# Kernel tuning notes

Measured on AMD Instinct MI355X. Metric: run time of the kernel, lower is better.

Reference implementation:

```python
import jax, jax.numpy as jnp
import numpy as np

# ---- static config (matches init_kwargs) ----
D_MODEL = 2048
D_STATE = 64
D_CONV = 4
EXPAND = 2
HEADDIM = 64
NGROUPS = 1
CHUNK = 256
D_INNER = EXPAND * D_MODEL            # 4096
NHEADS = D_INNER // HEADDIM           # 64
CONV_DIM = D_INNER + 2 * NGROUPS * D_STATE   # 4224
D_IN_PROJ = 2 * D_INNER + 2 * NGROUPS * D_STATE + NHEADS  # 8384
EPS = 1e-5


def setup_inputs() -> dict:
    key = jax.random.key(0)
    ks = jax.random.split(key, 7)
    B, L = 2, 2048
    u = jax.random.normal(ks[0], (B, L, D_MODEL), jnp.float32)
    W_in = jax.random.normal(ks[1], (D_IN_PROJ, D_MODEL), jnp.float32) * (D_MODEL ** -0.5)
    conv_w = jax.random.normal(ks[2], (CONV_DIM, D_CONV), jnp.float32) * (D_CONV ** -0.5)
    conv_b = jnp.zeros((CONV_DIM,), jnp.float32)
    # dt_bias = softplus^{-1}(dt) with dt ~ LogUniform(1e-3, 1e-1), as in the torch init
    dt = jnp.exp(jax.random.uniform(ks[3], (NHEADS,), jnp.float32)
                 * (np.log(0.1) - np.log(0.001)) + np.log(0.001))
    dt_bias = dt + jnp.log(-jnp.expm1(-dt))
    A_log = jnp.log(jax.random.uniform(ks[4], (NHEADS,), jnp.float32, minval=1.0, maxval=16.0))
    D = jnp.ones((NHEADS,), jnp.float32)
    norm_w = jnp.ones((D_INNER,), jnp.float32)
    W_out = jax.random.normal(ks[5], (D_MODEL, D_INNER), jnp.float32) * (D_INNER ** -0.5)
    return dict(u=u, W_in=W_in, conv_w=conv_w, conv_b=conv_b, dt_bias=dt_bias,
                A_log=A_log, D=D, norm_w=norm_w, W_out=W_out)


def _chunked_ssd(x, dt, A, Bm, Cm):
    """Mamba2 chunked selective scan (ssd, discrete form).
    x:[b,l,h,p] dt:[b,l,h] A:[h] Bm,Cm:[b,l,n] (ngroups=1, broadcast over heads).
    Returns y:[b,l,h,p]."""
    b, l, h, p = x.shape
    c = l // CHUNK
    xc = x.reshape(b, c, CHUNK, h, p)
    dtc = dt.reshape(b, c, CHUNK, h)
    Bc = Bm.reshape(b, c, CHUNK, D_STATE)
    Cc = Cm.reshape(b, c, CHUNK, D_STATE)

    Abar = (dtc * A).transpose(0, 3, 1, 2)          # [b,h,c,s]
    Acum = jnp.cumsum(Abar, axis=-1)                # [b,h,c,s]

    # intra-chunk decay matrix L[i,j] = exp(sum_{k=j+1..i} Abar_k), lower-tri
    seg = Acum[..., :, None] - Acum[..., None, :]   # [b,h,c,s,s]
    tri = jnp.tril(jnp.ones((CHUNK, CHUNK), bool))
    Lmat = jnp.where(tri, jnp.exp(seg), 0.0)

    xdt = xc * dtc[..., None]                       # [b,c,s,h,p] (dt*B*x discretization)
    Y_diag = jnp.einsum('bcln,bcsn,bhcls,bcshp->bclhp', Cc, Bc, Lmat, xdt)

    # per-chunk final states
    decay_states = jnp.exp(Acum[..., -1:] - Acum)   # [b,h,c,s]
    states = jnp.einsum('bcsn,bhcs,bcshp->bchpn', Bc, decay_states, xdt)

    # inter-chunk recurrence (associative scan across chunk summaries)
    Achunk = Acum[..., -1]                          # [b,h,c]
    Acs = jnp.cumsum(jnp.pad(Achunk, ((0, 0), (0, 0), (1, 0))), axis=-1)  # [b,h,c+1]
    segc = Acs[..., :, None] - Acs[..., None, :]
    tric = jnp.tril(jnp.ones((c + 1, c + 1), bool))
    decay_chunk = jnp.where(tric, jnp.exp(segc), 0.0)          # [b,h,c+1,c+1]
    states0 = jnp.pad(states, ((0, 0), (1, 0), (0, 0), (0, 0), (0, 0)))  # zero init state
    new_states = jnp.einsum('bhzc,bchpn->bzhpn', decay_chunk, states0)
    prev_states = new_states[:, :-1]                # state entering each chunk [b,c,h,p,n]

    state_decay = jnp.exp(Acum)                     # [b,h,c,s]
    Y_off = jnp.einsum('bcln,bchpn,bhcl->bclhp', Cc, prev_states, state_decay)
    return (Y_diag + Y_off).reshape(b, l, h, p)


def reference(u, W_in, conv_w, conv_b, dt_bias, A_log, D, norm_w, W_out):
    b, l, _ = u.shape
    zxbcdt = u @ W_in.T                                        # [b,l,8384]
    z = zxbcdt[..., :D_INNER]
    xBC = zxbcdt[..., D_INNER:D_INNER + CONV_DIM]
    dt = jax.nn.softplus(zxbcdt[..., D_INNER + CONV_DIM:] + dt_bias)  # [b,l,h]

    # causal depthwise conv1d + SiLU
    xp = jnp.pad(xBC, ((0, 0), (D_CONV - 1, 0), (0, 0)))
    xBC = conv_b + sum(xp[:, w:w + l, :] * conv_w[:, w] for w in range(D_CONV))
    xBC = jax.nn.silu(xBC)

    x = xBC[..., :D_INNER].reshape(b, l, NHEADS, HEADDIM)
    Bm = xBC[..., D_INNER:D_INNER + D_STATE]
    Cm = xBC[..., D_INNER + D_STATE:]

    A = -jnp.exp(A_log)                                        # [h]
    y = _chunked_ssd(x, dt, A, Bm, Cm)                         # [b,l,h,p]
    y = y + x * D[None, None, :, None]                         # D skip on raw x
    y = y.reshape(b, l, D_INNER)

    # gated RMSNorm (norm_before_gate=False): gate first, then normalize
    y = y * jax.nn.silu(z)
    y = y * jax.lax.rsqrt(jnp.mean(y * y, axis=-1, keepdims=True) + EPS) * norm_w
    return y @ W_out.T
```

## Files before the change

kernel.cpp:

```cpp
#include <hip/hip_runtime.h>
#include <hip/hip_bf16.h>
#include <cstdint>

#define DPROJ  8384

typedef __attribute__((ext_vector_type(8))) short short8;
typedef __attribute__((ext_vector_type(4))) short sh4;
typedef __attribute__((ext_vector_type(4))) float f32x4;

#define ZX16_OFF   0ul
#define DTB_OFF    17170432ul
#define ACU_OFF    17432576ul
#define CBT_OFF    17694720ul
#define ST_OFF     18219008ul
#define YB_OFF     22413312ul
#define HALO_OFF   39190528ul
#define U16_OFF    39393280ul
#define WIN16_OFF  43587584ul
#define WOUT16_OFF 39393280ul

__device__ __forceinline__ short f2bf(float x) {
  union { float f; uint32_t u; } v{x};
  uint32_t r = (v.u + 0x7fff + ((v.u >> 16) & 1)) >> 16;
  return (short)r;
}
__device__ __forceinline__ float bf2f(short s) {
  union { uint32_t u; float f; } v;
  v.u = ((uint32_t)(uint16_t)s) << 16;
  return v.f;
}

__global__ __launch_bounds__(256) void cast_bf16_kernel(
    const float* __restrict__ in, short* __restrict__ out, int n8) {
  int i = blockIdx.x * 256 + threadIdx.x;
  if (i >= n8) return;
  const float4* p = (const float4*)(in + (size_t)i * 8);
  float4 a = p[0], b = p[1];
  short8 o;
  o[0] = f2bf(a.x); o[1] = f2bf(a.y); o[2] = f2bf(a.z); o[3] = f2bf(a.w);
  o[4] = f2bf(b.x); o[5] = f2bf(b.y); o[6] = f2bf(b.z); o[7] = f2bf(b.w);
  *(short8*)(out + (size_t)i * 8) = o;
}

__device__ __forceinline__ void gload16(const void* g, const void* l) {
  __builtin_amdgcn_global_load_lds(
      (const __attribute__((address_space(1))) void*)g,
      (__attribute__((address_space(3))) void*)l, 16, 0, 0);
}

template <int OUTBF>
__global__ __launch_bounds__(256) void gemm_bf16(
    const short* __restrict__ A, int lda, const short* __restrict__ B, int ldb,
    void* __restrict__ Cv, int ldc, int K, int Nvalid) {
  const int orig = blockIdx.x + gridDim.x * blockIdx.y;
  const int xcd = orig & 7;
  const int cid = orig >> 3;
  const int rpx = gridDim.y >> 3;
  const int tn = cid / rpx;
  const int tm = xcd * rpx + (cid % rpx);
  __shared__ __align__(16) short As[128 * 32];
  __shared__ __align__(16) short Bs[128 * 32];
  const int t = threadIdx.x;
  const int w = t >> 6, lane = t & 63;
  const int m0 = tm * 128, n0 = tn * 128;
  const int wr = (w >> 1) * 64, wc = (w & 1) * 64;
  const int arow = t >> 2, kk = (t & 3) * 8;
  const int fr = lane & 15, fk = (lane >> 4) * 8;
  int br0 = n0 + arow;       if (br0 > Nvalid - 1) br0 = Nvalid - 1;
  int br1 = n0 + 64 + arow;  if (br1 > Nvalid - 1) br1 = Nvalid - 1;
  const short* pa0 = A + (size_t)(m0 + arow) * lda + kk;
  const short* pa1 = A + (size_t)(m0 + 64 + arow) * lda + kk;
  const short* pb0 = B + (size_t)br0 * ldb + kk;
  const short* pb1 = B + (size_t)br1 * ldb + kk;
  short* la = As + w * 512;
  short* lb = Bs + w * 512;
  f32x4 acc[4][4];
#pragma unroll
  for (int i = 0; i < 4; ++i)
#pragma unroll
    for (int j = 0; j < 4; ++j) acc[i][j] = (f32x4){0.f, 0.f, 0.f, 0.f};

  for (int k0 = 0; k0 < K; k0 += 32) {
    gload16(pa0 + k0, la);
    gload16(pa1 + k0, la + 2048);
    gload16(pb0 + k0, lb);
    gload16(pb1 + k0, lb + 2048);
    __syncthreads();
    short8 af[4], bg[4];
#pragma unroll
    for (int i = 0; i < 4; ++i) {
      af[i] = *(const short8*)&As[(wr + i * 16 + fr) * 32 + fk];
      bg[i] = *(const short8*)&Bs[(wc + i * 16 + fr) * 32 + fk];
    }
#pragma unroll
    for (int i = 0; i < 4; ++i)
#pragma unroll
      for (int j = 0; j < 4; ++j)
        acc[i][j] = __builtin_amdgcn_mfma_f32_16x16x32_bf16(af[i], bg[j],
                                                            acc[i][j], 0, 0, 0);
    __syncthreads();
  }
#pragma unroll
  for (int i = 0; i < 4; ++i) {
    const int row = m0 + wr + i * 16 + (lane >> 4) * 4;
#pragma unroll
    for (int j = 0; j < 4; ++j) {
      const int col = n0 + wc + j * 16 + fr;
      if (col < Nvalid) {
#pragma unroll
        for (int r = 0; r < 4; ++r) {
          if (OUTBF)
            ((short*)Cv)[(size_t)(row + r) * ldc + col] = f2bf(acc[i][j][r]);
          else
            ((float*)Cv)[(size_t)(row + r) * ldc + col] = acc[i][j][r];
        }
      }
    }
  }
}

__global__ __launch_bounds__(256) void halo_kernel(const short* __restrict__ zx,
                                                   short* __restrict__ halo) {
  int idx = blockIdx.x * 256 + threadIdx.x;
  int ch = idx % 4224;
  int r = idx / 4224;
  int j = r % 3;
  int r2 = r / 3;
  int lc = r2 & 15, b = r2 >> 4;
  int l = lc * 128 - 3 + j;
  halo[idx] = (l < 0) ? (short)0 : zx[(size_t)(b * 2048 + l) * DPROJ + 4096 + ch];
}

__global__ __launch_bounds__(256) void conv_kernel(short* __restrict__ zx,
                                                   const short* __restrict__ halo,
                                                   const float* __restrict__ cw,
                                                   const float* __restrict__ cb) {
  int idx = blockIdx.x * 256 + threadIdx.x;
  int ch = idx % 4224;
  int r = idx / 4224;
  int lc = r & 15, b = r >> 4;
  float w0 = cw[ch * 4 + 0], w1 = cw[ch * 4 + 1], w2 = cw[ch * 4 + 2],
        w3 = cw[ch * 4 + 3];
  float bias = cb[ch];
  const short* hp = halo + (size_t)r * 3 * 4224 + ch;
  float x3 = bf2f(hp[0]), x2 = bf2f(hp[4224]), x1 = bf2f(hp[2 * 4224]);
  size_t base = (size_t)(b * 2048 + lc * 128) * DPROJ + 4096 + ch;
  for (int i = 0; i < 128; ++i) {
    float x0 = bf2f(zx[base]);
    float v = bias + w0 * x3 + w1 * x2 + w2 * x1 + w3 * x0;
    v = v / (1.f + __expf(-v));
    zx[base] = f2bf(v);
    x3 = x2; x2 = x1; x1 = x0;
    base += DPROJ;
  }
}

__global__ __launch_bounds__(256) void dtacum_kernel(
    const short* __restrict__ zx, const float* __restrict__ dt_bias,
    const float* __restrict__ A_log, float* __restrict__ dtb,
    float* __restrict__ acu) {
  int bid = blockIdx.x;
  int c = bid & 7, h = (bid >> 3) & 63, b = bid >> 9;
  int s = threadIdx.x;
  int tok = b * 2048 + c * 256 + s;
  float raw = bf2f(zx[(size_t)tok * DPROJ + 8320 + h]) + dt_bias[h];
  float dtv = (raw > 20.f) ? raw : log1pf(expf(raw));
  float A = -expf(A_log[h]);
  __shared__ float sc[256];
  sc[s] = dtv * A;
  __syncthreads();
  for (int off = 1; off < 256; off <<= 1) {
    float v = (s >= off) ? sc[s - off] : 0.f;
    __syncthreads();
    sc[s] += v;
    __syncthreads();
  }
  int o = (b * 64 + h) * 2048 + c * 256 + s;
  dtb[o] = dtv;
  acu[o] = sc[s];
}

__global__ __launch_bounds__(256) void cbt_kernel(const short* __restrict__ zx,
                                                  short* __restrict__ cbtT) {
  __shared__ float cl[256][33];
  __shared__ float blds[16][32];
  int bid = blockIdx.x;
  int sb = bid & 15, c = (bid >> 4) & 7, b = bid >> 7;
  int t = threadIdx.x;
  int tok0 = b * 2048 + c * 256;
  float acc[16];
#pragma unroll
  for (int i = 0; i < 16; ++i) acc[i] = 0.f;
  for (int nh = 0; nh < 2; ++nh) {
    __syncthreads();
    for (int it = 0; it < 32; ++it) {
      int e = it * 256 + t;
      int row = e >> 5, n = e & 31;
      cl[row][n] = bf2f(zx[(size_t)(tok0 + row) * DPROJ + 8256 + nh * 32 + n]);
    }
    for (int it = 0; it < 2; ++it) {
      int e = it * 256 + t;
      int row = e >> 5, n = e & 31;
      blds[row][n] =
          bf2f(zx[(size_t)(tok0 + sb * 16 + row) * DPROJ + 8192 + nh * 32 + n]);
    }
    __syncthreads();
    for (int n = 0; n < 32; ++n) {
      float cv = cl[t][n];
#pragma unroll
      for (int s2 = 0; s2 < 16; ++s2) acc[s2] += cv * blds[s2][n];
    }
  }
  short* outp = cbtT + ((size_t)(b * 8 + c) * 256 + t) * 256 + sb * 16;
#pragma unroll
  for (int s2 = 0; s2 < 16; ++s2) outp[s2] = f2bf(acc[s2]);
}

__global__ __launch_bounds__(256) void states_mfma(
    const short* __restrict__ zx, const float* __restrict__ dtb,
    const float* __restrict__ acu, float* __restrict__ st) {
  __shared__ __align__(16) short As2[64][136];
  __shared__ __align__(16) short Bs2[64][136];
  __shared__ float wl[256];
  int bid = blockIdx.x;
  int h = bid & 63, c = (bid >> 6) & 7, b = bid >> 9;
  int t = threadIdx.x;
  int w = t >> 6, lane = t & 63;
  int tok0 = b * 2048 + c * 256;
  int bh = (b * 64 + h) * 2048 + c * 256;
  {
    float aend = acu[bh + 255];
    wl[t] = __expf(aend - acu[bh + t]) * dtb[bh + t];
  }
  __syncthreads();
  const short* xbase = zx + (size_t)tok0 * DPROJ + 4096 + h * 64;
  const short* bbase = zx + (size_t)tok0 * DPROJ + 8192;
  const int fr = lane & 15, fko = (lane >> 4) * 8;
  const int wi = (w >> 1) * 32, wj = (w & 1) * 32;
  f32x4 acc[2][2];
#pragma unroll
  for (int i = 0; i < 2; ++i)
#pragma unroll
    for (int j = 0; j < 2; ++j) acc[i][j] = (f32x4){0.f, 0.f, 0.f, 0.f};

  for (int ph = 0; ph < 2; ++ph) {
    const int kb = ph * 128;
    if (ph) __syncthreads();
    for (int it = 0; it < 8; ++it) {
      int idx = it * 256 + t;
      int p = idx & 63, kg = idx >> 6;
      int k = kb + kg * 4;
      const short* xp = xbase + (size_t)k * DPROJ + p;
      const short* bp = bbase + (size_t)k * DPROJ + p;
      sh4 oa, ob;
#pragma unroll
      for (int r = 0; r < 4; ++r) {
        oa[r] = xp[(size_t)r * DPROJ];
        ob[r] = f2bf(bf2f(bp[(size_t)r * DPROJ]) * wl[k + r]);
      }
      *(sh4*)&As2[p][kg * 4] = oa;
      *(sh4*)&Bs2[p][kg * 4] = ob;
    }
    __syncthreads();
#pragma unroll
    for (int kk0 = 0; kk0 < 128; kk0 += 32) {
      short8 af[2], bg[2];
#pragma unroll
      for (int i = 0; i < 2; ++i) {
        af[i] = *(const short8*)&As2[wi + i * 16 + fr][kk0 + fko];
        bg[i] = *(const short8*)&Bs2[wj + i * 16 + fr][kk0 + fko];
      }
#pragma unroll
      for (int i = 0; i < 2; ++i)
#pragma unroll
        for (int j = 0; j < 2; ++j)
          acc[i][j] = __builtin_amdgcn_mfma_f32_16x16x32_bf16(af[i], bg[j],
                                                              acc[i][j], 0, 0, 0);
    }
  }
  float* out = st + ((size_t)(b * 8 + c) * 64 + h) * 4096;
  const int rq = (lane >> 4) * 4;
#pragma unroll
  for (int i = 0; i < 2; ++i) {
    int p0 = wi + i * 16 + rq;
#pragma unroll
    for (int j = 0; j < 2; ++j) {
      int n = wj + j * 16 + fr;
#pragma unroll
      for (int r = 0; r < 4; ++r)
        out[(size_t)(p0 + r) * 64 + n] = acc[i][j][r];
    }
  }
}

__global__ __launch_bounds__(256) void chunkscan_kernel(
    const float* __restrict__ acu, float* __restrict__ st) {
  int bid = blockIdx.x;
  int pc = bid & 15, h = (bid >> 4) & 63, b = bid >> 10;
  int pn = pc * 256 + threadIdx.x;
  int abase = (b * 64 + h) * 2048;
  float run = 0.f;
  for (int c = 0; c < 8; ++c) {
    size_t idx = ((size_t)(b * 8 + c) * 64 + h) * 4096 + pn;
    float s = st[idx];
    st[idx] = run;
    float ach = acu[abase + c * 256 + 255];
    run = run * __expf(ach) + s;
  }
}

__global__ __launch_bounds__(256) void ydiag_mfma(
    const short* __restrict__ zx, const float* __restrict__ dtb,
    const float* __restrict__ acu, const short* __restrict__ cbtT,
    const float* __restrict__ st, const float* __restrict__ Dp,
    float* __restrict__ yb) {
  __shared__ __align__(16) short Xs[64][328];
  __shared__ float acs[256];
  __shared__ float dts[256];
  int bid = blockIdx.x;
  int h = bid & 63, c = (bid >> 6) & 7, b = bid >> 9;
  int t = threadIdx.x;
  int w = t >> 6, lane = t & 63;
  int tok0 = b * 2048 + c * 256;
  int bh = (b * 64 + h) * 2048 + c * 256;
  acs[t] = acu[bh + t];
  dts[t] = dtb[bh + t];
  const short* xbase = zx + (size_t)tok0 * DPROJ + 4096 + h * 64;
  const float* st_b = st + ((size_t)(b * 8 + c) * 64 + h) * 4096;
  for (int it = 0; it < 16; ++it) {
    int idx = it * 256 + t;
    int p = idx & 63, kg = idx >> 6;
    const short* xp = xbase + (size_t)(kg * 4) * DPROJ + p;
    sh4 o;
    o[0] = xp[0];
    o[1] = xp[DPROJ];
    o[2] = xp[2 * DPROJ];
    o[3] = xp[3 * DPROJ];
    *(sh4*)&Xs[p][kg * 4] = o;
  }
  for (int it = 0; it < 4; ++it) {
    int idx = it * 256 + t;
    int ng = idx & 15, p = idx >> 4;
    float4 v = *(const float4*)&st_b[p * 64 + ng * 4];
    sh4 o;
    o[0] = f2bf(v.x); o[1] = f2bf(v.y); o[2] = f2bf(v.z); o[3] = f2bf(v.w);
    *(sh4*)&Xs[p][256 + ng * 4] = o;
  }
  __syncthreads();

  const int fr = lane & 15, fko = (lane >> 4) * 8;
  const int wr = w * 64;
  float Al[4], eAl[4];
#pragma unroll
  for (int i = 0; i < 4; ++i) {
    Al[i] = acs[wr + i * 16 + fr];
    eAl[i] = __expf(Al[i]);
  }
  f32x4 acc[4][4];
#pragma unroll
  for (int i = 0; i < 4; ++i)
#pragma unroll
    for (int j = 0; j < 4; ++j) acc[i][j] = (f32x4){0.f, 0.f, 0.f, 0.f};

  const short* cbt_b = cbtT + (size_t)(b * 8 + c) * 65536;

  for (int k0 = 0; k0 < wr + 64; k0 += 32) {
    short8 bg[4];
#pragma unroll
    for (int j = 0; j < 4; ++j)
      bg[j] = *(const short8*)&Xs[j * 16 + fr][k0 + fko];
    const int bi = (k0 + 32 < 256) ? (k0 + 32) : 255;
    const float base = acs[bi];
    float vd[8];
#pragma unroll
    for (int jj = 0; jj < 8; ++jj) {
      int s = k0 + fko + jj;
      vd[jj] = __expf(base - acs[s]) * dts[s];
    }
#pragma unroll
    for (int i = 0; i < 4; ++i) {
      const int li0 = wr + i * 16;
      if (k0 > li0 + 15) continue;
      const int l = li0 + fr;
      const short8 cb = *(const short8*)&cbt_b[(size_t)l * 256 + k0 + fko];
      short8 af;
      if (k0 + 32 <= li0) {
        const float u = __expf(Al[i] - base);
#pragma unroll
        for (int jj = 0; jj < 8; ++jj)
          af[jj] = f2bf(bf2f(cb[jj]) * (vd[jj] * u));
      } else {
#pragma unroll
        for (int jj = 0; jj < 8; ++jj) {
          int s = k0 + fko + jj;
          float wv = 0.f;
          if (s <= l) wv = bf2f(cb[jj]) * __expf(Al[i] - acs[s]) * dts[s];
          af[jj] = f2bf(wv);
        }
      }
#pragma unroll
      for (int j = 0; j < 4; ++j)
        acc[i][j] = __builtin_amdgcn_mfma_f32_16x16x32_bf16(af, bg[j],
                                                            acc[i][j], 0, 0, 0);
    }
  }
#pragma unroll
  for (int k0 = 256; k0 < 320; k0 += 32) {
    short8 bg[4];
#pragma unroll
    for (int j = 0; j < 4; ++j)
      bg[j] = *(const short8*)&Xs[j * 16 + fr][k0 + fko];
#pragma unroll
    for (int i = 0; i < 4; ++i) {
      const int l = wr + i * 16 + fr;
      const short8 cv = *(const short8*)(zx + (size_t)(tok0 + l) * DPROJ +
                                         8256 + (k0 - 256) + fko);
      short8 af;
#pragma unroll
      for (int jj = 0; jj < 8; ++jj) af[jj] = f2bf(bf2f(cv[jj]) * eAl[i]);
#pragma unroll
      for (int j = 0; j < 4; ++j)
        acc[i][j] = __builtin_amdgcn_mfma_f32_16x16x32_bf16(af, bg[j],
                                                            acc[i][j], 0, 0, 0);
    }
  }
  float Dh = Dp[h];
  const int rq = (lane >> 4) * 4;
#pragma unroll
  for (int i = 0; i < 4; ++i) {
    int l0 = wr + i * 16 + rq;
#pragma unroll
    for (int j = 0; j < 4; ++j) {
      int p = j * 16 + fr;
      sh4 x4 = *(const sh4*)&Xs[p][l0];
      f32x4 a = acc[i][j];
#pragma unroll
      for (int r = 0; r < 4; ++r)
        yb[(size_t)(bh + l0 + r) * 64 + p] = a[r] + Dh * bf2f(x4[r]);
    }
  }
}

__global__ __launch_bounds__(256) void gatenorm_kernel(
    short* zx, const float* __restrict__ nw, const float* __restrict__ yb) {
  int tok = blockIdx.x;
  int b = tok >> 11, l = tok & 2047;
  int t = threadIdx.x;
  float g[16];
  float ss = 0.f;
#pragma unroll
  for (int i = 0; i < 16; ++i) {
    int d = i * 256 + t;
    int h = d >> 6, p = d & 63;
    float yv = yb[((size_t)(b * 64 + h) * 2048 + l) * 64 + p];
    float zv = bf2f(zx[(size_t)tok * DPROJ + d]);
    float gv = yv * (zv / (1.f + __expf(-zv)));
    g[i] = gv;
    ss += gv * gv;
  }
  for (int off = 32; off > 0; off >>= 1) ss += __shfl_down(ss, off);
  __shared__ float red[4];
  int wid = t >> 6, lane = t & 63;
  if (lane == 0) red[wid] = ss;
  __syncthreads();
  float tot = red[0] + red[1] + red[2] + red[3];
  float scale = rsqrtf(tot * (1.f / 4096.f) + 1e-5f);
#pragma unroll
  for (int i = 0; i < 16; ++i) {
    int d = i * 256 + t;
    zx[(size_t)tok * DPROJ + d] = f2bf(g[i] * scale * nw[d]);
  }
}

extern "C" void kernel_launch(void* const* d_in, const int* in_sizes, int n_in,
                              void* d_out, int out_size, void* d_ws,
                              size_t ws_size, hipStream_t stream) {
  const float* u = (const float*)d_in[0];
  const float* W_in = (const float*)d_in[1];
  const float* conv_w = (const float*)d_in[2];
  const float* conv_b = (const float*)d_in[3];
  const float* dt_bias = (const float*)d_in[4];
  const float* A_log = (const float*)d_in[5];
  const float* Dp = (const float*)d_in[6];
  const float* norm_w = (const float*)d_in[7];
  const float* W_out = (const float*)d_in[8];
  float* out = (float*)d_out;
  float* ws = (float*)d_ws;

  short* zx16 = (short*)(ws + ZX16_OFF);
  float* dtb = ws + DTB_OFF;
  float* acu = ws + ACU_OFF;
  short* cbtT = (short*)(ws + CBT_OFF);
  float* st = ws + ST_OFF;
  float* yb = ws + YB_OFF;
  short* halo = (short*)(ws + HALO_OFF);
  short* u16 = (short*)(ws + U16_OFF);
  short* win16 = (short*)(ws + WIN16_OFF);
  short* wout16 = (short*)(ws + WOUT16_OFF);

  cast_bf16_kernel<<<4096, 256, 0, stream>>>(u, u16, 1048576);
  cast_bf16_kernel<<<8384, 256, 0, stream>>>(W_in, win16, 2146304);
  gemm_bf16<1><<<dim3(66, 32), 256, 0, stream>>>(u16, 2048, win16, 2048, zx16,
                                                 DPROJ, 2048, DPROJ);
  halo_kernel<<<1584, 256, 0, stream>>>(zx16, halo);
  conv_kernel<<<528, 256, 0, stream>>>(zx16, halo, conv_w, conv_b);
  dtacum_kernel<<<1024, 256, 0, stream>>>(zx16, dt_bias, A_log, dtb, acu);
  cbt_kernel<<<256, 256, 0, stream>>>(zx16, cbtT);
  states_mfma<<<1024, 256, 0, stream>>>(zx16, dtb, acu, st);
  chunkscan_kernel<<<2048, 256, 0, stream>>>(acu, st);
  ydiag_mfma<<<1024, 256, 0, stream>>>(zx16, dtb, acu, cbtT, st, Dp, yb);
  cast_bf16_kernel<<<4096, 256, 0, stream>>>(W_out, wout16, 1048576);
  gatenorm_kernel<<<4096, 256, 0, stream>>>(zx16, norm_w, yb);
  gemm_bf16<0><<<dim3(16, 32), 256, 0, stream>>>(zx16, DPROJ, wout16, 4096, out,
                                                 2048, 4096, 2048);
}
```

Baseline: 485.1 us.

## Double GEMM K-tile to 64 with XOR-swizzled LDS; store y intermediate as bf16

The bf16 GEMM now loads a 64-wide K slice per iteration into LDS using an XOR swizzle on 16-byte chunks. This halves the number of barrier pairs per K loop and is meant to reduce LDS bank conflicts on fragment reads, at the cost of twice the shared memory per block. Separately, the SSD output buffer between ydiag and gatenorm is stored as bf16 instead of fp32. That halves its write and read traffic but adds rounding error before the RMSNorm.

```diff
diff --git a/kernel.cpp b/kernel.cpp
--- a/kernel.cpp
+++ b/kernel.cpp
@@ -58,46 +58,58 @@
   const int rpx = gridDim.y >> 3;
   const int tn = cid / rpx;
   const int tm = xcd * rpx + (cid % rpx);
-  __shared__ __align__(16) short As[128 * 32];
-  __shared__ __align__(16) short Bs[128 * 32];
+  __shared__ __align__(16) short As[128 * 64];
+  __shared__ __align__(16) short Bs[128 * 64];
   const int t = threadIdx.x;
   const int w = t >> 6, lane = t & 63;
   const int m0 = tm * 128, n0 = tn * 128;
   const int wr = (w >> 1) * 64, wc = (w & 1) * 64;
-  const int arow = t >> 2, kk = (t & 3) * 8;
-  const int fr = lane & 15, fk = (lane >> 4) * 8;
-  int br0 = n0 + arow;       if (br0 > Nvalid - 1) br0 = Nvalid - 1;
-  int br1 = n0 + 64 + arow;  if (br1 > Nvalid - 1) br1 = Nvalid - 1;
-  const short* pa0 = A + (size_t)(m0 + arow) * lda + kk;
-  const short* pa1 = A + (size_t)(m0 + 64 + arow) * lda + kk;
-  const short* pb0 = B + (size_t)br0 * ldb + kk;
-  const short* pb1 = B + (size_t)br1 * ldb + kk;
-  short* la = As + w * 512;
-  short* lb = Bs + w * 512;
+  const int fr = lane & 15;
+  const int cik = lane >> 4;
+  const int frs = fr & 7;
+  const int rl = lane >> 3;
+  const int sch = ((lane & 7) ^ rl) << 3;
+  const short* pa_[4];
+  const short* pb_[4];
+#pragma unroll
+  for (int c = 0; c < 4; ++c) {
+    int r = c * 32 + w * 8 + rl;
+    pa_[c] = A + (size_t)(m0 + r) * lda + sch;
+    int br = n0 + r;
+    if (br > Nvalid - 1) br = Nvalid - 1;
+    pb_[c] = B + (size_t)br * ldb + sch;
+  }
   f32x4 acc[4][4];
 #pragma unroll
   for (int i = 0; i < 4; ++i)
 #pragma unroll
     for (int j = 0; j < 4; ++j) acc[i][j] = (f32x4){0.f, 0.f, 0.f, 0.f};
 
-  for (int k0 = 0; k0 < K; k0 += 32) {
-    gload16(pa0 + k0, la);
-    gload16(pa1 + k0, la + 2048);
-    gload16(pb0 + k0, lb);
-    gload16(pb1 + k0, lb + 2048);
-    __syncthreads();
-    short8 af[4], bg[4];
-#pragma unroll
-    for (int i = 0; i < 4; ++i) {
-      af[i] = *(const short8*)&As[(wr + i * 16 + fr) * 32 + fk];
-      bg[i] = *(const short8*)&Bs[(wc + i * 16 + fr) * 32 + fk];
-    }
-#pragma unroll
-    for (int i = 0; i < 4; ++i)
-#pragma unroll
-      for (int j = 0; j < 4; ++j)
-        acc[i][j] = __builtin_amdgcn_mfma_f32_16x16x32_bf16(af[i], bg[j],
-                                                            acc[i][j], 0, 0, 0);
+  for (int k0 = 0; k0 < K; k0 += 64) {
+#pragma unroll
+    for (int c = 0; c < 4; ++c) {
+      gload16(pa_[c] + k0, &As[c * 2048 + w * 512 + lane * 8]);
+      gload16(pb_[c] + k0, &Bs[c * 2048 + w * 512 + lane * 8]);
+    }
+    __syncthreads();
+#pragma unroll
+    for (int kk = 0; kk < 2; ++kk) {
+      const int ci = kk * 4 + cik;
+      short8 af[4], bg[4];
+#pragma unroll
+      for (int i = 0; i < 4; ++i) {
+        const int ra = wr + i * 16 + fr;
+        const int rb = wc + i * 16 + fr;
+        af[i] = *(const short8*)&As[ra * 64 + ((ci ^ frs) << 3)];
+        bg[i] = *(const short8*)&Bs[rb * 64 + ((ci ^ frs) << 3)];
+      }
+#pragma unroll
+      for (int i = 0; i < 4; ++i)
+#pragma unroll
+        for (int j = 0; j < 4; ++j)
+          acc[i][j] = __builtin_amdgcn_mfma_f32_16x16x32_bf16(af[i], bg[j],
+                                                              acc[i][j], 0, 0, 0);
+    }
     __syncthreads();
   }
 #pragma unroll
@@ -313,7 +325,7 @@
     const short* __restrict__ zx, const float* __restrict__ dtb,
     const float* __restrict__ acu, const short* __restrict__ cbtT,
     const float* __restrict__ st, const float* __restrict__ Dp,
-    float* __restrict__ yb) {
+    short* __restrict__ yb) {
   __shared__ __align__(16) short Xs[64][328];
   __shared__ float acs[256];
   __shared__ float dts[256];
@@ -436,13 +448,13 @@
       f32x4 a = acc[i][j];
 #pragma unroll
       for (int r = 0; r < 4; ++r)
-        yb[(size_t)(bh + l0 + r) * 64 + p] = a[r] + Dh * bf2f(x4[r]);
+        yb[(size_t)(bh + l0 + r) * 64 + p] = f2bf(a[r] + Dh * bf2f(x4[r]));
     }
   }
 }
 
 __global__ __launch_bounds__(256) void gatenorm_kernel(
-    short* zx, const float* __restrict__ nw, const float* __restrict__ yb) {
+    short* zx, const float* __restrict__ nw, const short* __restrict__ yb) {
   int tok = blockIdx.x;
   int b = tok >> 11, l = tok & 2047;
   int t = threadIdx.x;
@@ -452,7 +464,7 @@
   for (int i = 0; i < 16; ++i) {
     int d = i * 256 + t;
     int h = d >> 6, p = d & 63;
-    float yv = yb[((size_t)(b * 64 + h) * 2048 + l) * 64 + p];
+    float yv = bf2f(yb[((size_t)(b * 64 + h) * 2048 + l) * 64 + p]);
     float zv = bf2f(zx[(size_t)tok * DPROJ + d]);
     float gv = yv * (zv / (1.f + __expf(-zv)));
     g[i] = gv;
@@ -492,7 +504,7 @@
   float* acu = ws + ACU_OFF;
   short* cbtT = (short*)(ws + CBT_OFF);
   float* st = ws + ST_OFF;
-  float* yb = ws + YB_OFF;
+  short* yb = (short*)(ws + YB_OFF);
   short* halo = (short*)(ws + HALO_OFF);
   short* u16 = (short*)(ws + U16_OFF);
   short* win16 = (short*)(ws + WIN16_OFF);
```

Result: faster. 444.5 us (-8.4%).
